# Performance work log

Measured on AMD Instinct MI355X. Metric: run time of the kernel, lower is better.

Reference implementation:

```python
import jax, jax.numpy as jnp
import numpy as np

B, S, D, C = 8, 2048, 1024, 4096

def setup_inputs() -> dict:
    key = jax.random.key(0)
    k1, k2 = jax.random.split(key)
    x = jax.random.normal(k1, (B, S, D), dtype=jnp.float32)
    label_repr = jax.random.normal(k2, (C, D), dtype=jnp.float32)
    return {"x": x, "label_repr": label_repr}

def reference(x, label_repr):
    # A = softmax(x @ label_repr^T) over label axis: [B,S,C]
    scores = jnp.einsum('bsd,cd->bsc', x, label_repr)
    A = jax.nn.softmax(scores, axis=-1)
    # output = A^T @ x : [B,C,D]
    output = jnp.einsum('bsc,bsd->bcd', A, x)
    return (output, A)
```

## Files before the change

### kernel.cpp

```cpp
#include <hip/hip_runtime.h>
#include <hip/hip_bf16.h>

#define NB 8
#define NS 2048
#define ND 1024
#define NC 4096
#define NM (NB*NS)

typedef __attribute__((ext_vector_type(8))) short bf16x8;
typedef __attribute__((ext_vector_type(4))) float floatx4;

__device__ __forceinline__ unsigned short f2bf(float f) {
  unsigned int u = __builtin_bit_cast(unsigned int, f);
  u += 0x7fffu + ((u >> 16) & 1u);
  return (unsigned short)(u >> 16);
}
__device__ __forceinline__ float bf2f(unsigned short h) {
  unsigned int u = ((unsigned int)h) << 16;
  return __builtin_bit_cast(float, u);
}

__global__ __launch_bounds__(256, 2)
void gemm1_scores(const float* __restrict__ x, const float* __restrict__ L,
                  float* __restrict__ sc) {
  __shared__ unsigned short sAh[128*40];
  __shared__ unsigned short sAl[128*40];
  __shared__ unsigned short sBh[128*40];
  __shared__ unsigned short sBl[128*40];
  const int tid = threadIdx.x;
  const int m0 = blockIdx.y << 7;
  const int n0 = blockIdx.x << 7;
  const int w  = tid >> 6;
  const int l  = tid & 63;
  const int wm = (w >> 1) << 6;
  const int wn = (w & 1) << 6;
  const int lrow = l & 15;
  const int quad = l >> 4;

  floatx4 acc[4][4] = {};

  const int srow = tid >> 3;
  const int scol = (tid & 7) << 2;

  const float* xa = x + (size_t)(m0 + srow) * ND + scol;
  const float* lb = L + (size_t)(n0 + srow) * ND + scol;

  for (int k0 = 0; k0 < ND; k0 += 32) {
    float4 av[4], bv[4];
    #pragma unroll
    for (int p = 0; p < 4; ++p) {
      av[p] = *(const float4*)(xa + (size_t)(p*32) * ND + k0);
      bv[p] = *(const float4*)(lb + (size_t)(p*32) * ND + k0);
    }
    __syncthreads();
    #pragma unroll
    for (int p = 0; p < 4; ++p) {
      const int r = srow + p*32;
      ushort4 h, lo;
      h.x = f2bf(av[p].x); lo.x = f2bf(av[p].x - bf2f(h.x));
      h.y = f2bf(av[p].y); lo.y = f2bf(av[p].y - bf2f(h.y));
      h.z = f2bf(av[p].z); lo.z = f2bf(av[p].z - bf2f(h.z));
      h.w = f2bf(av[p].w); lo.w = f2bf(av[p].w - bf2f(h.w));
      *(ushort4*)&sAh[r*40 + scol] = h;
      *(ushort4*)&sAl[r*40 + scol] = lo;
      h.x = f2bf(bv[p].x); lo.x = f2bf(bv[p].x - bf2f(h.x));
      h.y = f2bf(bv[p].y); lo.y = f2bf(bv[p].y - bf2f(h.y));
      h.z = f2bf(bv[p].z); lo.z = f2bf(bv[p].z - bf2f(h.z));
      h.w = f2bf(bv[p].w); lo.w = f2bf(bv[p].w - bf2f(h.w));
      *(ushort4*)&sBh[r*40 + scol] = h;
      *(ushort4*)&sBl[r*40 + scol] = lo;
    }
    __syncthreads();
    bf16x8 ah[4], bh[4], t[4];
    #pragma unroll
    for (int i = 0; i < 4; ++i) ah[i] = *(const bf16x8*)&sAh[(wm + i*16 + lrow)*40 + quad*8];
    #pragma unroll
    for (int j = 0; j < 4; ++j) bh[j] = *(const bf16x8*)&sBh[(wn + j*16 + lrow)*40 + quad*8];
    #pragma unroll
    for (int i = 0; i < 4; ++i)
      #pragma unroll
      for (int j = 0; j < 4; ++j)
        acc[i][j] = __builtin_amdgcn_mfma_f32_16x16x32_bf16(ah[i], bh[j], acc[i][j], 0, 0, 0);
    #pragma unroll
    for (int i = 0; i < 4; ++i) t[i] = *(const bf16x8*)&sAl[(wm + i*16 + lrow)*40 + quad*8];
    #pragma unroll
    for (int i = 0; i < 4; ++i)
      #pragma unroll
      for (int j = 0; j < 4; ++j)
        acc[i][j] = __builtin_amdgcn_mfma_f32_16x16x32_bf16(t[i], bh[j], acc[i][j], 0, 0, 0);
    #pragma unroll
    for (int j = 0; j < 4; ++j) t[j] = *(const bf16x8*)&sBl[(wn + j*16 + lrow)*40 + quad*8];
    #pragma unroll
    for (int i = 0; i < 4; ++i)
      #pragma unroll
      for (int j = 0; j < 4; ++j)
        acc[i][j] = __builtin_amdgcn_mfma_f32_16x16x32_bf16(ah[i], t[j], acc[i][j], 0, 0, 0);
  }

  float* op = sc + (size_t)(m0 + wm + quad*4) * NC + (n0 + wn + lrow);
  #pragma unroll
  for (int i = 0; i < 4; ++i)
    #pragma unroll
    for (int r = 0; r < 4; ++r)
      #pragma unroll
      for (int j = 0; j < 4; ++j)
        op[(size_t)(i*16 + r) * NC + j*16] = acc[i][j][r];
}

__global__ __launch_bounds__(256)
void softmax_rows(float* __restrict__ A) {
  float* row = A + (size_t)blockIdx.x * NC;
  const int tid = threadIdx.x;
  float4 v[4];
  float mx = -3.0e38f;
  #pragma unroll
  for (int i = 0; i < 4; ++i) {
    v[i] = *(const float4*)(row + (tid << 2) + (i << 10));
    mx = fmaxf(mx, fmaxf(fmaxf(v[i].x, v[i].y), fmaxf(v[i].z, v[i].w)));
  }
  #pragma unroll
  for (int off = 32; off > 0; off >>= 1) mx = fmaxf(mx, __shfl_xor(mx, off));
  __shared__ float red[4];
  if ((tid & 63) == 0) red[tid >> 6] = mx;
  __syncthreads();
  mx = fmaxf(fmaxf(red[0], red[1]), fmaxf(red[2], red[3]));
  float s = 0.f;
  #pragma unroll
  for (int i = 0; i < 4; ++i) {
    v[i].x = __expf(v[i].x - mx); v[i].y = __expf(v[i].y - mx);
    v[i].z = __expf(v[i].z - mx); v[i].w = __expf(v[i].w - mx);
    s += (v[i].x + v[i].y) + (v[i].z + v[i].w);
  }
  #pragma unroll
  for (int off = 32; off > 0; off >>= 1) s += __shfl_xor(s, off);
  __syncthreads();
  if ((tid & 63) == 0) red[tid >> 6] = s;
  __syncthreads();
  s = (red[0] + red[1]) + (red[2] + red[3]);
  const float inv = 1.0f / s;
  #pragma unroll
  for (int i = 0; i < 4; ++i) {
    v[i].x *= inv; v[i].y *= inv; v[i].z *= inv; v[i].w *= inv;
    *(float4*)(row + (tid << 2) + (i << 10)) = v[i];
  }
}

__global__ __launch_bounds__(256, 2)
void gemm2_out(const float* __restrict__ A, const float* __restrict__ x,
               float* __restrict__ out) {
  __shared__ unsigned short sA[128*40];
  __shared__ unsigned short sX[128*40];
  const int tid = threadIdx.x;
  const float* Ab = A + (size_t)blockIdx.z * NS * NC;
  const float* xb = x + (size_t)blockIdx.z * NS * ND;
  float* ob = out + (size_t)blockIdx.z * NC * ND;
  const int m0 = blockIdx.y << 7;
  const int n0 = blockIdx.x << 7;
  const int w  = tid >> 6;
  const int l  = tid & 63;
  const int wm = (w >> 1) << 6;
  const int wn = (w & 1) << 6;
  const int lrow = l & 15;
  const int quad = l >> 4;

  floatx4 acc[4][4] = {};

  const int sp0 = tid & 15;
  const int cg0 = tid >> 4;

  for (int k0 = 0; k0 < NS; k0 += 32) {
    float4 a[2][2], xv[2][2];
    const int s = k0 + sp0*2;
    #pragma unroll
    for (int p = 0; p < 2; ++p) {
      const int c4 = (cg0 + p*16) << 2;
      a[p][0]  = *(const float4*)(Ab + (size_t)s     * NC + m0 + c4);
      a[p][1]  = *(const float4*)(Ab + (size_t)(s+1) * NC + m0 + c4);
      xv[p][0] = *(const float4*)(xb + (size_t)s     * ND + n0 + c4);
      xv[p][1] = *(const float4*)(xb + (size_t)(s+1) * ND + n0 + c4);
    }
    __syncthreads();
    #pragma unroll
    for (int p = 0; p < 2; ++p) {
      const int c4 = (cg0 + p*16) << 2;
      const float* fa0 = (const float*)&a[p][0];
      const float* fa1 = (const float*)&a[p][1];
      const float* fx0 = (const float*)&xv[p][0];
      const float* fx1 = (const float*)&xv[p][1];
      #pragma unroll
      for (int i = 0; i < 4; ++i) {
        const unsigned int pa = (unsigned int)f2bf(fa0[i]) | ((unsigned int)f2bf(fa1[i]) << 16);
        const unsigned int px = (unsigned int)f2bf(fx0[i]) | ((unsigned int)f2bf(fx1[i]) << 16);
        *(unsigned int*)&sA[(c4 + i)*40 + sp0*2] = pa;
        *(unsigned int*)&sX[(c4 + i)*40 + sp0*2] = px;
      }
    }
    __syncthreads();
    bf16x8 af[4], bg[4];
    #pragma unroll
    for (int i = 0; i < 4; ++i) af[i] = *(const bf16x8*)&sA[(wm + i*16 + lrow)*40 + quad*8];
    #pragma unroll
    for (int j = 0; j < 4; ++j) bg[j] = *(const bf16x8*)&sX[(wn + j*16 + lrow)*40 + quad*8];
    #pragma unroll
    for (int i = 0; i < 4; ++i)
      #pragma unroll
      for (int j = 0; j < 4; ++j)
        acc[i][j] = __builtin_amdgcn_mfma_f32_16x16x32_bf16(af[i], bg[j], acc[i][j], 0, 0, 0);
  }

  float* op = ob + (size_t)(m0 + wm + quad*4) * ND + (n0 + wn + lrow);
  #pragma unroll
  for (int i = 0; i < 4; ++i)
    #pragma unroll
    for (int r = 0; r < 4; ++r)
      #pragma unroll
      for (int j = 0; j < 4; ++j)
        op[(size_t)(i*16 + r) * ND + j*16] = acc[i][j][r];
}

extern "C" void kernel_launch(void* const* d_in, const int* in_sizes, int n_in,
                              void* d_out, int out_size, void* d_ws, size_t ws_size,
                              hipStream_t stream) {
  const float* x = (const float*)d_in[0];
  const float* L = (const float*)d_in[1];
  float* out = (float*)d_out;
  float* A   = out + (size_t)NB * NC * ND;

  gemm1_scores<<<dim3(NC/128, NM/128), 256, 0, stream>>>(x, L, A);
  softmax_rows<<<dim3(NM), 256, 0, stream>>>(A);
  gemm2_out<<<dim3(ND/128, NC/128, NB), 256, 0, stream>>>(A, x, out);
}
```

Before: 1.352 ms.

## Pre-split inputs to bf16 hi/lo in workspace and stream tiles via global_load_lds

Adds prep kernels that convert L and x once into bf16 hi/lo split arrays plus a transposed bf16 copy of x in workspace. The softmax now also writes a transposed bf16 copy of A. Both GEMMs load pre-converted bf16 tiles straight into LDS with global_load_lds instead of loading fp32 and converting in registers per tile. The aim is to cut the repeated per-tile conversion and halve GEMM operand bandwidth. In exchange it adds extra passes and workspace traffic, and the operand LDS tiles lose their row padding, which may cause bank conflicts.

```diff
diff --git a/kernel.cpp b/kernel.cpp
--- a/kernel.cpp
+++ b/kernel.cpp
@@ -9,6 +9,7 @@
 
 typedef __attribute__((ext_vector_type(8))) short bf16x8;
 typedef __attribute__((ext_vector_type(4))) float floatx4;
+typedef unsigned short ushort_t;
 
 __device__ __forceinline__ unsigned short f2bf(float f) {
   unsigned int u = __builtin_bit_cast(unsigned int, f);
@@ -19,6 +20,271 @@
   unsigned int u = ((unsigned int)h) << 16;
   return __builtin_bit_cast(float, u);
 }
+
+__device__ __forceinline__ void load_lds16(const void* g, void* s) {
+  __builtin_amdgcn_global_load_lds(
+      (const __attribute__((address_space(1))) char*)g,
+      (__attribute__((address_space(3))) char*)s, 16, 0, 0);
+}
+
+
+__global__ __launch_bounds__(256)
+void prep_L(const float* __restrict__ L, ushort_t* __restrict__ Lh,
+            ushort_t* __restrict__ Ll) {
+  const size_t i = ((size_t)blockIdx.x * 256 + threadIdx.x) * 4;
+  float4 v = *(const float4*)(L + i);
+  ushort4 h, lo;
+  h.x = f2bf(v.x); lo.x = f2bf(v.x - bf2f(h.x));
+  h.y = f2bf(v.y); lo.y = f2bf(v.y - bf2f(h.y));
+  h.z = f2bf(v.z); lo.z = f2bf(v.z - bf2f(h.z));
+  h.w = f2bf(v.w); lo.w = f2bf(v.w - bf2f(h.w));
+  *(ushort4*)(Lh + i) = h;
+  *(ushort4*)(Ll + i) = lo;
+}
+
+__global__ __launch_bounds__(256)
+void prep_x(const float* __restrict__ x, ushort_t* __restrict__ xh,
+            ushort_t* __restrict__ xl, ushort_t* __restrict__ xT) {
+  __shared__ unsigned int tile[256 * 17];
+  const int b = blockIdx.z;
+  const int s0 = blockIdx.y << 5;
+  const int d0 = blockIdx.x << 8;
+  const int tid = threadIdx.x;
+  const int sp = tid & 15, cg = tid >> 4;
+  const int r0 = 2 * sp, r1 = r0 + 1;
+  const float* xb = x + (size_t)b * NS * ND;
+  ushort_t* xhb = xh + (size_t)b * NS * ND;
+  ushort_t* xlb = xl + (size_t)b * NS * ND;
+  #pragma unroll
+  for (int i = 0; i < 4; ++i) {
+    const int crel = cg * 4 + i * 64;
+    const int col = d0 + crel;
+    float4 v0 = *(const float4*)(xb + (size_t)(s0 + r0) * ND + col);
+    float4 v1 = *(const float4*)(xb + (size_t)(s0 + r1) * ND + col);
+    ushort4 h0, l0, h1, l1;
+    h0.x = f2bf(v0.x); l0.x = f2bf(v0.x - bf2f(h0.x));
+    h0.y = f2bf(v0.y); l0.y = f2bf(v0.y - bf2f(h0.y));
+    h0.z = f2bf(v0.z); l0.z = f2bf(v0.z - bf2f(h0.z));
+    h0.w = f2bf(v0.w); l0.w = f2bf(v0.w - bf2f(h0.w));
+    h1.x = f2bf(v1.x); l1.x = f2bf(v1.x - bf2f(h1.x));
+    h1.y = f2bf(v1.y); l1.y = f2bf(v1.y - bf2f(h1.y));
+    h1.z = f2bf(v1.z); l1.z = f2bf(v1.z - bf2f(h1.z));
+    h1.w = f2bf(v1.w); l1.w = f2bf(v1.w - bf2f(h1.w));
+    *(ushort4*)(xhb + (size_t)(s0 + r0) * ND + col) = h0;
+    *(ushort4*)(xlb + (size_t)(s0 + r0) * ND + col) = l0;
+    *(ushort4*)(xhb + (size_t)(s0 + r1) * ND + col) = h1;
+    *(ushort4*)(xlb + (size_t)(s0 + r1) * ND + col) = l1;
+    tile[(crel + 0) * 17 + sp] = (unsigned)h0.x | ((unsigned)h1.x << 16);
+    tile[(crel + 1) * 17 + sp] = (unsigned)h0.y | ((unsigned)h1.y << 16);
+    tile[(crel + 2) * 17 + sp] = (unsigned)h0.z | ((unsigned)h1.z << 16);
+    tile[(crel + 3) * 17 + sp] = (unsigned)h0.w | ((unsigned)h1.w << 16);
+  }
+  __syncthreads();
+  unsigned tmp[16];
+  #pragma unroll
+  for (int k = 0; k < 16; ++k) tmp[k] = tile[tid * 17 + k];
+  ushort_t* dst = xT + ((size_t)b * ND + d0 + tid) * NS + s0;
+  #pragma unroll
+  for (int k = 0; k < 4; ++k) *(uint4*)(dst + k * 8) = *(uint4*)&tmp[k * 4];
+}
+
+__global__ __launch_bounds__(256, 2)
+void gemm1_v2(const ushort_t* __restrict__ xh, const ushort_t* __restrict__ xl,
+              const ushort_t* __restrict__ Lh, const ushort_t* __restrict__ Ll,
+              float* __restrict__ sc) {
+  __shared__ ushort_t sAh[128 * 32];
+  __shared__ ushort_t sAl[128 * 32];
+  __shared__ ushort_t sBh[128 * 32];
+  __shared__ ushort_t sBl[128 * 32];
+  const int tid = threadIdx.x;
+  const int m0 = blockIdx.y << 7;
+  const int n0 = blockIdx.x << 7;
+  const int w = tid >> 6, l = tid & 63;
+  const int wm = (w >> 1) << 6;
+  const int wn = (w & 1) << 6;
+  const int lrow = l & 15, quad = l >> 4;
+  const int srow = l >> 2;
+  const int skol = (l & 3) << 3;
+
+  floatx4 acc[4][4] = {};
+
+  for (int k0 = 0; k0 < ND; k0 += 32) {
+    __syncthreads();
+    #pragma unroll
+    for (int q = 0; q < 2; ++q) {
+      const int row = w * 32 + q * 16 + srow;
+      const size_t ga = (size_t)(m0 + row) * ND + k0 + skol;
+      const size_t gb = (size_t)(n0 + row) * ND + k0 + skol;
+      const int lo = w * 1024 + q * 512;
+      load_lds16(xh + ga, &sAh[lo]);
+      load_lds16(xl + ga, &sAl[lo]);
+      load_lds16(Lh + gb, &sBh[lo]);
+      load_lds16(Ll + gb, &sBl[lo]);
+    }
+    __syncthreads();
+    bf16x8 ah[4], bh[4], t[4];
+    #pragma unroll
+    for (int i = 0; i < 4; ++i) ah[i] = *(const bf16x8*)&sAh[(wm + i*16 + lrow)*32 + quad*8];
+    #pragma unroll
+    for (int j = 0; j < 4; ++j) bh[j] = *(const bf16x8*)&sBh[(wn + j*16 + lrow)*32 + quad*8];
+    #pragma unroll
+    for (int i = 0; i < 4; ++i)
+      #pragma unroll
+      for (int j = 0; j < 4; ++j)
+        acc[i][j] = __builtin_amdgcn_mfma_f32_16x16x32_bf16(ah[i], bh[j], acc[i][j], 0, 0, 0);
+    #pragma unroll
+    for (int i = 0; i < 4; ++i) t[i] = *(const bf16x8*)&sAl[(wm + i*16 + lrow)*32 + quad*8];
+    #pragma unroll
+    for (int i = 0; i < 4; ++i)
+      #pragma unroll
+      for (int j = 0; j < 4; ++j)
+        acc[i][j] = __builtin_amdgcn_mfma_f32_16x16x32_bf16(t[i], bh[j], acc[i][j], 0, 0, 0);
+    #pragma unroll
+    for (int j = 0; j < 4; ++j) t[j] = *(const bf16x8*)&sBl[(wn + j*16 + lrow)*32 + quad*8];
+    #pragma unroll
+    for (int i = 0; i < 4; ++i)
+      #pragma unroll
+      for (int j = 0; j < 4; ++j)
+        acc[i][j] = __builtin_amdgcn_mfma_f32_16x16x32_bf16(ah[i], t[j], acc[i][j], 0, 0, 0);
+  }
+
+  float* op = sc + (size_t)(m0 + wm + quad * 4) * NC + (n0 + wn + lrow);
+  #pragma unroll
+  for (int i = 0; i < 4; ++i)
+    #pragma unroll
+    for (int r = 0; r < 4; ++r)
+      #pragma unroll
+      for (int j = 0; j < 4; ++j)
+        op[(size_t)(i * 16 + r) * NC + j * 16] = acc[i][j][r];
+}
+
+__global__ __launch_bounds__(256)
+void softmax_T(float* __restrict__ A, ushort_t* __restrict__ AT) {
+  __shared__ float sm[32], sli[32];
+  __shared__ unsigned int tile[256 * 17];
+  const int s0 = blockIdx.x << 5;
+  const int b = s0 >> 11;
+  const int sl0 = s0 & (NS - 1);
+  const int tid = threadIdx.x;
+  const int w = tid >> 6, l = tid & 63;
+
+  float m[8], su[8];
+  #pragma unroll
+  for (int r = 0; r < 8; ++r) { m[r] = -3.0e38f; su[r] = 0.f; }
+  for (int ch = 0; ch < 16; ++ch) {
+    #pragma unroll
+    for (int r = 0; r < 8; ++r) {
+      float4 v = *(const float4*)(A + (size_t)(s0 + w * 8 + r) * NC + ch * 256 + (l << 2));
+      float mx = fmaxf(fmaxf(v.x, v.y), fmaxf(v.z, v.w));
+      float nm = fmaxf(m[r], mx);
+      su[r] = su[r] * __expf(m[r] - nm) +
+              __expf(v.x - nm) + __expf(v.y - nm) + __expf(v.z - nm) + __expf(v.w - nm);
+      m[r] = nm;
+    }
+  }
+  #pragma unroll
+  for (int r = 0; r < 8; ++r) {
+    #pragma unroll
+    for (int off = 32; off; off >>= 1) {
+      float om = __shfl_xor(m[r], off);
+      float os = __shfl_xor(su[r], off);
+      float nm = fmaxf(m[r], om);
+      su[r] = su[r] * __expf(m[r] - nm) + os * __expf(om - nm);
+      m[r] = nm;
+    }
+    if (l == 0) { sm[w * 8 + r] = m[r]; sli[w * 8 + r] = 1.0f / su[r]; }
+  }
+  __syncthreads();
+
+  const int sp = tid & 15, cg = tid >> 4;
+  const int r0 = 2 * sp, r1 = r0 + 1;
+  const float M0 = sm[r0], I0 = sli[r0];
+  const float M1 = sm[r1], I1 = sli[r1];
+  float* A0 = A + (size_t)(s0 + r0) * NC;
+  float* A1 = A + (size_t)(s0 + r1) * NC;
+  for (int ch = 0; ch < 16; ++ch) {
+    const int cb = ch << 8;
+    #pragma unroll
+    for (int i = 0; i < 4; ++i) {
+      const int crel = cg * 4 + i * 64;
+      float4 v0 = *(const float4*)(A0 + cb + crel);
+      float4 v1 = *(const float4*)(A1 + cb + crel);
+      float4 p0, p1;
+      p0.x = __expf(v0.x - M0) * I0; p0.y = __expf(v0.y - M0) * I0;
+      p0.z = __expf(v0.z - M0) * I0; p0.w = __expf(v0.w - M0) * I0;
+      p1.x = __expf(v1.x - M1) * I1; p1.y = __expf(v1.y - M1) * I1;
+      p1.z = __expf(v1.z - M1) * I1; p1.w = __expf(v1.w - M1) * I1;
+      *(float4*)(A0 + cb + crel) = p0;
+      *(float4*)(A1 + cb + crel) = p1;
+      tile[(crel + 0) * 17 + sp] = (unsigned)f2bf(p0.x) | ((unsigned)f2bf(p1.x) << 16);
+      tile[(crel + 1) * 17 + sp] = (unsigned)f2bf(p0.y) | ((unsigned)f2bf(p1.y) << 16);
+      tile[(crel + 2) * 17 + sp] = (unsigned)f2bf(p0.z) | ((unsigned)f2bf(p1.z) << 16);
+      tile[(crel + 3) * 17 + sp] = (unsigned)f2bf(p0.w) | ((unsigned)f2bf(p1.w) << 16);
+    }
+    __syncthreads();
+    unsigned tmp[16];
+    #pragma unroll
+    for (int k = 0; k < 16; ++k) tmp[k] = tile[tid * 17 + k];
+    ushort_t* dst = AT + ((size_t)b * NC + cb + tid) * NS + sl0;
+    #pragma unroll
+    for (int k = 0; k < 4; ++k) *(uint4*)(dst + k * 8) = *(uint4*)&tmp[k * 4];
+    __syncthreads();
+  }
+}
+
+__global__ __launch_bounds__(256, 2)
+void gemm2_v2(const ushort_t* __restrict__ AT, const ushort_t* __restrict__ xT,
+              float* __restrict__ out) {
+  __shared__ ushort_t sA[128 * 32];
+  __shared__ ushort_t sX[128 * 32];
+  const int tid = threadIdx.x;
+  const int b = blockIdx.z;
+  const ushort_t* Ab = AT + (size_t)b * NC * NS;
+  const ushort_t* xb = xT + (size_t)b * ND * NS;
+  float* ob = out + (size_t)b * NC * ND;
+  const int m0 = blockIdx.y << 7;
+  const int n0 = blockIdx.x << 7;
+  const int w = tid >> 6, l = tid & 63;
+  const int wm = (w >> 1) << 6;
+  const int wn = (w & 1) << 6;
+  const int lrow = l & 15, quad = l >> 4;
+  const int srow = l >> 2;
+  const int skol = (l & 3) << 3;
+
+  floatx4 acc[4][4] = {};
+
+  for (int k0 = 0; k0 < NS; k0 += 32) {
+    __syncthreads();
+    #pragma unroll
+    for (int q = 0; q < 2; ++q) {
+      const int row = w * 32 + q * 16 + srow;
+      const int lo = w * 1024 + q * 512;
+      load_lds16(Ab + (size_t)(m0 + row) * NS + k0 + skol, &sA[lo]);
+      load_lds16(xb + (size_t)(n0 + row) * NS + k0 + skol, &sX[lo]);
+    }
+    __syncthreads();
+    bf16x8 af[4], bg[4];
+    #pragma unroll
+    for (int i = 0; i < 4; ++i) af[i] = *(const bf16x8*)&sA[(wm + i*16 + lrow)*32 + quad*8];
+    #pragma unroll
+    for (int j = 0; j < 4; ++j) bg[j] = *(const bf16x8*)&sX[(wn + j*16 + lrow)*32 + quad*8];
+    #pragma unroll
+    for (int i = 0; i < 4; ++i)
+      #pragma unroll
+      for (int j = 0; j < 4; ++j)
+        acc[i][j] = __builtin_amdgcn_mfma_f32_16x16x32_bf16(af[i], bg[j], acc[i][j], 0, 0, 0);
+  }
+
+  float* op = ob + (size_t)(m0 + wm + quad * 4) * ND + (n0 + wn + lrow);
+  #pragma unroll
+  for (int i = 0; i < 4; ++i)
+    #pragma unroll
+    for (int r = 0; r < 4; ++r)
+      #pragma unroll
+      for (int j = 0; j < 4; ++j)
+        op[(size_t)(i * 16 + r) * ND + j * 16] = acc[i][j][r];
+}
+
 
 __global__ __launch_bounds__(256, 2)
 void gemm1_scores(const float* __restrict__ x, const float* __restrict__ L,
@@ -36,15 +302,11 @@
   const int wn = (w & 1) << 6;
   const int lrow = l & 15;
   const int quad = l >> 4;
-
   floatx4 acc[4][4] = {};
-
   const int srow = tid >> 3;
   const int scol = (tid & 7) << 2;
-
   const float* xa = x + (size_t)(m0 + srow) * ND + scol;
   const float* lb = L + (size_t)(n0 + srow) * ND + scol;
-
   for (int k0 = 0; k0 < ND; k0 += 32) {
     float4 av[4], bv[4];
     #pragma unroll
@@ -96,7 +358,6 @@
       for (int j = 0; j < 4; ++j)
         acc[i][j] = __builtin_amdgcn_mfma_f32_16x16x32_bf16(ah[i], t[j], acc[i][j], 0, 0, 0);
   }
-
   float* op = sc + (size_t)(m0 + wm + quad*4) * NC + (n0 + wn + lrow);
   #pragma unroll
   for (int i = 0; i < 4; ++i)
@@ -162,12 +423,9 @@
   const int wn = (w & 1) << 6;
   const int lrow = l & 15;
   const int quad = l >> 4;
-
   floatx4 acc[4][4] = {};
-
   const int sp0 = tid & 15;
   const int cg0 = tid >> 4;
-
   for (int k0 = 0; k0 < NS; k0 += 32) {
     float4 a[2][2], xv[2][2];
     const int s = k0 + sp0*2;
@@ -207,7 +465,6 @@
       for (int j = 0; j < 4; ++j)
         acc[i][j] = __builtin_amdgcn_mfma_f32_16x16x32_bf16(af[i], bg[j], acc[i][j], 0, 0, 0);
   }
-
   float* op = ob + (size_t)(m0 + wm + quad*4) * ND + (n0 + wn + lrow);
   #pragma unroll
   for (int i = 0; i < 4; ++i)
@@ -217,6 +474,7 @@
       for (int j = 0; j < 4; ++j)
         op[(size_t)(i*16 + r) * ND + j*16] = acc[i][j][r];
 }
+
 
 extern "C" void kernel_launch(void* const* d_in, const int* in_sizes, int n_in,
                               void* d_out, int out_size, void* d_ws, size_t ws_size,
@@ -226,7 +484,26 @@
   float* out = (float*)d_out;
   float* A   = out + (size_t)NB * NC * ND;
 
-  gemm1_scores<<<dim3(NC/128, NM/128), 256, 0, stream>>>(x, L, A);
-  softmax_rows<<<dim3(NM), 256, 0, stream>>>(A);
-  gemm2_out<<<dim3(ND/128, NC/128, NB), 256, 0, stream>>>(A, x, out);
-}
+  const size_t EL_X  = (size_t)NB * NS * ND;
+  const size_t EL_L  = (size_t)NC * ND;
+  const size_t EL_AT = (size_t)NB * NC * NS;
+  const size_t need  = (3 * EL_X + 2 * EL_L + EL_AT) * sizeof(ushort_t);
+
+  if (ws_size >= need) {
+    ushort_t* xh = (ushort_t*)d_ws;
+    ushort_t* xl = xh + EL_X;
+    ushort_t* xT = xl + EL_X;
+    ushort_t* Lh = xT + EL_X;
+    ushort_t* Ll = Lh + EL_L;
+    ushort_t* AT = Ll + EL_L;
+    prep_L<<<dim3((NC * ND) / 1024), 256, 0, stream>>>(L, Lh, Ll);
+    prep_x<<<dim3(ND / 256, NS / 32, NB), 256, 0, stream>>>(x, xh, xl, xT);
+    gemm1_v2<<<dim3(NC / 128, NM / 128), 256, 0, stream>>>(xh, xl, Lh, Ll, A);
+    softmax_T<<<dim3(NM / 32), 256, 0, stream>>>(A, AT);
+    gemm2_v2<<<dim3(ND / 128, NC / 128, NB), 256, 0, stream>>>(AT, xT, out);
+  } else {
+    gemm1_scores<<<dim3(NC / 128, NM / 128), 256, 0, stream>>>(x, L, A);
+    softmax_rows<<<dim3(NM), 256, 0, stream>>>(A);
+    gemm2_out<<<dim3(ND / 128, NC / 128, NB), 256, 0, stream>>>(A, x, out);
+  }
+}
```

After: 1.166 ms. 13.8% less time.
